# Kernel tuning notes

Measured on AMD Instinct MI355X. Metric: run time of the kernel, lower is better.

Reference implementation:

```python
import jax, jax.numpy as jnp
import numpy as np

D_MODEL = 1024
N_HEADS = 16
D_HEAD = D_MODEL // N_HEADS
ROPE_BASE = 10000.0


def _rotate_half(x):
    half = x.shape[-1] // 2
    x1, x2 = x[..., :half], x[..., half:]
    return jnp.concatenate([-x2, x1], axis=-1)


def _rope_cos_sin(seq_len, d_head, dtype):
    inv_freq = 1.0 / (ROPE_BASE ** (jnp.arange(0, d_head, 2, dtype=jnp.float32) / d_head))
    t = jnp.arange(seq_len, dtype=jnp.float32)
    freqs = jnp.outer(t, inv_freq)                       # [S, d_head/2]
    emb = jnp.concatenate([freqs, freqs], axis=-1)       # [S, d_head]
    return jnp.cos(emb).astype(dtype), jnp.sin(emb).astype(dtype)


def setup_inputs() -> dict:
    key = jax.random.key(0)
    k1, k2, k3 = jax.random.split(key, 3)
    B, S = 2, 2048
    x = jax.random.normal(k1, (B, S, D_MODEL), dtype=jnp.float32)
    # torch nn.Linear weight layout: [out_features, in_features], y = x @ W.T
    w_qkv = jax.random.normal(k2, (3 * D_MODEL, D_MODEL), dtype=jnp.float32) * (D_MODEL ** -0.5)
    w_out = jax.random.normal(k3, (D_MODEL, D_MODEL), dtype=jnp.float32) * (D_MODEL ** -0.5)
    return {"x": x, "w_qkv": w_qkv, "w_out": w_out}


def reference(x, w_qkv, w_out):
    B, S, _ = x.shape
    qkv = jnp.einsum('bsd,ed->bse', x, w_qkv)            # [B, S, 3*D]
    qkv = qkv.reshape(B, S, 3, N_HEADS, D_HEAD)
    qkv = jnp.transpose(qkv, (2, 0, 3, 1, 4))            # [3, B, H, S, Dh]
    q, k, v = qkv[0], qkv[1], qkv[2]

    cos, sin = _rope_cos_sin(S, D_HEAD, x.dtype)         # [S, Dh] each
    cos = cos[None, None]                                # [1, 1, S, Dh]
    sin = sin[None, None]
    q = q * cos + _rotate_half(q) * sin
    k = k * cos + _rotate_half(k) * sin

    scale = 1.0 / jnp.sqrt(jnp.array(D_HEAD, dtype=x.dtype))
    attn = jnp.einsum('bhqd,bhkd->bhqk', q, k) * scale   # [B, H, S, S]
    causal = jnp.tril(jnp.ones((S, S), dtype=bool))      # triu(diag=1) masked -> keep lower tri
    attn = jnp.where(causal[None, None], attn, jnp.finfo(x.dtype).min)
    attn = jax.nn.softmax(attn, axis=-1)

    out = jnp.einsum('bhqk,bhkd->bhqd', attn, v)         # [B, H, S, Dh]
    out = jnp.transpose(out, (0, 2, 1, 3)).reshape(B, S, D_MODEL)
    return jnp.einsum('bsd,ed->bse', out, w_out)         # out_proj
```

## Files before the change

### kernel.cpp

```cpp
#include <hip/hip_runtime.h>
#include <hip/hip_bf16.h>
#include <cmath>

#define DMODEL 1024
#define NH 16
#define DH 64
#define SEQ 2048
#define BATCH 2

typedef __attribute__((ext_vector_type(8))) short bf16x8;
typedef __attribute__((ext_vector_type(4))) float f32x4;
typedef __attribute__((ext_vector_type(4))) unsigned int u32x4;
typedef __attribute__((ext_vector_type(8))) unsigned short u16x8;

__device__ __forceinline__ unsigned short f2bf(float f) {
    unsigned int u = __builtin_bit_cast(unsigned int, f);
    u += 0x7fffu + ((u >> 16) & 1u);
    return (unsigned short)(u >> 16);
}
__device__ __forceinline__ float exp2_fast(float x) {
    float r;
    asm("v_exp_f32 %0, %1" : "=v"(r) : "v"(x));
    return r;
}

__global__ __launch_bounds__(256)
void cast_all(const float* __restrict__ x, const float* __restrict__ wq,
              const float* __restrict__ wo, unsigned short* __restrict__ xb,
              unsigned short* __restrict__ wqb, unsigned short* __restrict__ wob)
{
    const int i = blockIdx.x * 256 + threadIdx.x;
    const float* src; unsigned short* dst; int off;
    if (i < 524288)      { src = x;  dst = xb;  off = i; }
    else if (i < 917504) { src = wq; dst = wqb; off = i - 524288; }
    else                 { src = wo; dst = wob; off = i - 917504; }
    const float4 a = *(const float4*)(src + (size_t)off * 8);
    const float4 b = *(const float4*)(src + (size_t)off * 8 + 4);
    u16x8 o;
    o[0] = f2bf(a.x); o[1] = f2bf(a.y); o[2] = f2bf(a.z); o[3] = f2bf(a.w);
    o[4] = f2bf(b.x); o[5] = f2bf(b.y); o[6] = f2bf(b.z); o[7] = f2bf(b.w);
    *(u16x8*)(dst + (size_t)off * 8) = o;
}

template<int BM, int EPI>
__global__ __launch_bounds__(256)
void gemm_bf16(const unsigned short* __restrict__ A,
               const unsigned short* __restrict__ B,
               float* __restrict__ oc, unsigned short* __restrict__ oq,
               unsigned short* __restrict__ ok, unsigned short* __restrict__ ovt,
               int M, int N)
{
    constexpr int K = 1024;
    constexpr int BK = 32;
    constexpr int NT = K / BK;
    constexpr int FM = BM / 32;
    __shared__ unsigned short As[2][BM * BK];
    __shared__ unsigned short Bs[2][128 * BK];

    const int t  = threadIdx.x;
    const int l  = t & 63;
    const int w  = t >> 6;
    const int g  = l >> 4;
    const int ln = l & 15;
    const int wr = w >> 1, wc = w & 1;
    const int m0 = blockIdx.y * BM;
    const int n0 = blockIdx.x * 128;

    auto stage = [&](int kt, int bufi) {
        #pragma unroll
        for (int i = 0; i < BM / 64; ++i) {
            const int n = i * 256 + t;
            const int r = n >> 2, slot = n & 3;
            const int kk = kt * BK + ((slot ^ ((r >> 1) & 3)) * 8);
            const unsigned short* ga = A + (size_t)(m0 + r) * K + kk;
            __builtin_amdgcn_global_load_lds(
                (const __attribute__((address_space(1))) unsigned int*)ga,
                (__attribute__((address_space(3))) unsigned int*)&As[bufi][n * 8], 16, 0, 0);
        }
        #pragma unroll
        for (int i = 0; i < 2; ++i) {
            const int n = i * 256 + t;
            const int r = n >> 2, slot = n & 3;
            const int kk = kt * BK + ((slot ^ ((r >> 1) & 3)) * 8);
            const unsigned short* gb = B + (size_t)(n0 + r) * K + kk;
            __builtin_amdgcn_global_load_lds(
                (const __attribute__((address_space(1))) unsigned int*)gb,
                (__attribute__((address_space(3))) unsigned int*)&Bs[bufi][n * 8], 16, 0, 0);
        }
    };

    f32x4 acc[FM][4];
    #pragma unroll
    for (int i = 0; i < FM; ++i)
        #pragma unroll
        for (int j = 0; j < 4; ++j) acc[i][j] = (f32x4){0.f, 0.f, 0.f, 0.f};

    const int swz = (g ^ ((ln >> 1) & 3)) << 4;

    stage(0, 0);
    for (int kt = 0; kt < NT; ++kt) {
        __syncthreads();
        if (kt + 1 < NT) stage(kt + 1, (kt + 1) & 1);
        const char* as = (const char*)As[kt & 1];
        const char* bs = (const char*)Bs[kt & 1];
        bf16x8 af[FM], bfr[4];
        #pragma unroll
        for (int fm = 0; fm < FM; ++fm)
            af[fm] = *(const bf16x8*)(as + (wr * (BM / 2) + fm * 16 + ln) * 64 + swz);
        #pragma unroll
        for (int fn = 0; fn < 4; ++fn)
            bfr[fn] = *(const bf16x8*)(bs + (wc * 64 + fn * 16 + ln) * 64 + swz);
        #pragma unroll
        for (int fm = 0; fm < FM; ++fm)
            #pragma unroll
            for (int fn = 0; fn < 4; ++fn)
                acc[fm][fn] = __builtin_amdgcn_mfma_f32_16x16x32_bf16(
                    af[fm], bfr[fn], acc[fm][fn], 0, 0, 0);
    }

    const int rowbase = m0 + wr * (BM / 2);
    const int colbase = n0 + wc * 64;
    if (EPI == 1) {
        #pragma unroll
        for (int fm = 0; fm < FM; ++fm)
            #pragma unroll
            for (int fn = 0; fn < 4; ++fn)
                #pragma unroll
                for (int rr = 0; rr < 4; ++rr) {
                    const int row = rowbase + fm * 16 + g * 4 + rr;
                    oc[(size_t)row * N + colbase + fn * 16 + ln] = acc[fm][fn][rr];
                }
    } else {
        const int which = colbase >> 10;
        const int h = (colbase >> 6) & (NH - 1);
        if (which < 2) {
            unsigned short* dst = which == 0 ? oq : ok;
            const float scale = which == 0 ? 0.18033688011112042f : 1.f;
            const float cexp = -13.287712379549449f / 32.f;
            const float if0 = exp2f((float)ln * cexp);
            const float if1 = exp2f((float)(16 + ln) * cexp);
            #pragma unroll
            for (int fm = 0; fm < FM; ++fm)
                #pragma unroll
                for (int rr = 0; rr < 4; ++rr) {
                    const int row = rowbase + fm * 16 + g * 4 + rr;
                    const int b = row >> 11, s = row & (SEQ - 1);
                    float s0, c0, s1, c1;
                    __sincosf((float)s * if0, &s0, &c0);
                    __sincosf((float)s * if1, &s1, &c1);
                    const float x0 = acc[fm][0][rr], x1 = acc[fm][1][rr];
                    const float x2 = acc[fm][2][rr], x3 = acc[fm][3][rr];
                    const size_t base = (((size_t)b * NH + h) * SEQ + s) * DH;
                    dst[base + ln]      = f2bf((x0 * c0 - x2 * s0) * scale);
                    dst[base + 16 + ln] = f2bf((x1 * c1 - x3 * s1) * scale);
                    dst[base + 32 + ln] = f2bf((x2 * c0 + x0 * s0) * scale);
                    dst[base + 48 + ln] = f2bf((x3 * c1 + x1 * s1) * scale);
                }
        } else {
            #pragma unroll
            for (int fm = 0; fm < FM; ++fm)
                #pragma unroll
                for (int fn = 0; fn < 4; ++fn) {
                    const int row = rowbase + fm * 16 + g * 4;
                    const int b = row >> 11, s = row & (SEQ - 1);
                    const int d = fn * 16 + ln;
                    ushort4 pk;
                    pk.x = f2bf(acc[fm][fn][0]); pk.y = f2bf(acc[fm][fn][1]);
                    pk.z = f2bf(acc[fm][fn][2]); pk.w = f2bf(acc[fm][fn][3]);
                    *(ushort4*)&ovt[(((size_t)b * NH + h) * DH + d) * SEQ + s] = pk;
                }
        }
    }
}

__global__ __launch_bounds__(512)
void attn_mfma(const unsigned short* __restrict__ q,
               const unsigned short* __restrict__ k,
               const unsigned short* __restrict__ vt,
               unsigned short* __restrict__ ob)
{
    __shared__ unsigned short Ks[2][64 * 64];
    __shared__ unsigned short Vs[2][64 * 64];

    const int t  = threadIdx.x;
    const int l  = t & 63;
    const int w  = t >> 6;
    const int wq = w & 3;
    const int g  = l >> 4;
    const int ln = l & 15;
    const int bid = blockIdx.x;
    const int xcd = bid & 7, jj = bid >> 3;
    const int bh = xcd * 4 + (jj >> 4);
    const int pi = jj & 15;
    const int qtA = pi, qtB = 31 - pi;
    const int myqt = (w < 4) ? qtA : qtB;
    const size_t bqk = (size_t)bh * SEQ * DH;
    const size_t bv  = (size_t)bh * DH * SEQ;

    bf16x8 qf0, qf1;
    {
        const unsigned short* qp = q + bqk + (size_t)(myqt * 64 + wq * 16 + ln) * DH + g * 8;
        qf0 = *(const bf16x8*)qp;
        qf1 = *(const bf16x8*)(qp + 32);
    }

    f32x4 ao[4];
    #pragma unroll
    for (int i = 0; i < 4; ++i) ao[i] = (f32x4){0.f, 0.f, 0.f, 0.f};
    float l_ = 0.f;

    auto stage = [&](int kt, int bufi) {
        const int row = t >> 3, sl = t & 7;
        const int sg  = (row & 3) | (((row >> 3) & 1) << 2);
        const int slg = (sl ^ sg) * 8;
        const unsigned short* gk = k  + bqk + (size_t)(kt * 64 + row) * DH + slg;
        const unsigned short* gv = vt + bv  + (size_t)row * SEQ + kt * 64 + slg;
        __builtin_amdgcn_global_load_lds(
            (const __attribute__((address_space(1))) unsigned int*)gk,
            (__attribute__((address_space(3))) unsigned int*)&Ks[bufi][t * 8], 16, 0, 0);
        __builtin_amdgcn_global_load_lds(
            (const __attribute__((address_space(1))) unsigned int*)gv,
            (__attribute__((address_space(3))) unsigned int*)&Vs[bufi][t * 8], 16, 0, 0);
    };

    const int rowoffK = ((ln >> 2) * 8 + (ln & 3)) * 128;
    const int sK = (ln & 3) | (((ln >> 2) & 1) << 2);
    const int slotK0 = ((g ^ sK) << 4);
    const int slotK1 = (((g + 4) ^ sK) << 4);
    const int sV = (ln & 3) | (((ln >> 3) & 1) << 2);

    stage(0, 0);
    for (int kt = 0; kt <= qtB; ++kt) {
        __syncthreads();
        if (kt < qtB) stage(kt + 1, (kt + 1) & 1);
        const bool act = (kt <= myqt);
        const char* kb = (const char*)Ks[kt & 1];
        const char* vb = (const char*)Vs[kt & 1];

        if (act) {
            f32x4 s[4];
            #pragma unroll
            for (int nb = 0; nb < 4; ++nb) s[nb] = (f32x4){0.f, 0.f, 0.f, 0.f};

            __builtin_amdgcn_s_setprio(1);
            #pragma unroll
            for (int nb = 0; nb < 4; ++nb) {
                const char* kr = kb + ((nb >> 1) * 32 + (nb & 1) * 4) * 128 + rowoffK;
                bf16x8 kf0 = *(const bf16x8*)(kr + slotK0);
                bf16x8 kf1 = *(const bf16x8*)(kr + slotK1);
                s[nb] = __builtin_amdgcn_mfma_f32_16x16x32_bf16(kf0, qf0, s[nb], 0, 0, 0);
                s[nb] = __builtin_amdgcn_mfma_f32_16x16x32_bf16(kf1, qf1, s[nb], 0, 0, 0);
            }
            __builtin_amdgcn_s_setprio(0);

            if (kt == myqt) {
                #pragma unroll
                for (int nb = 0; nb < 4; ++nb)
                    #pragma unroll
                    for (int r = 0; r < 4; ++r)
                        if ((nb >> 1) * 32 + g * 8 + (nb & 1) * 4 + r > wq * 16 + ln)
                            s[nb][r] = -INFINITY;
            }

            const float M2 = 28.853900817779268f;
            bf16x8 pf[2];
            {
                float rs = 0.f;
                unsigned int dw[8];
                #pragma unroll
                for (int nb = 0; nb < 4; ++nb) {
                    float e[4];
                    #pragma unroll
                    for (int r = 0; r < 4; ++r)
                        e[r] = exp2_fast(s[nb][r] - M2);
                    rs += (e[0] + e[1]) + (e[2] + e[3]);
                    dw[nb * 2] = __builtin_amdgcn_perm(
                        __builtin_bit_cast(unsigned int, e[1]),
                        __builtin_bit_cast(unsigned int, e[0]), 0x07060302u);
                    dw[nb * 2 + 1] = __builtin_amdgcn_perm(
                        __builtin_bit_cast(unsigned int, e[3]),
                        __builtin_bit_cast(unsigned int, e[2]), 0x07060302u);
                }
                l_ += rs;
                pf[0] = __builtin_bit_cast(bf16x8, (u32x4){dw[0], dw[1], dw[2], dw[3]});
                pf[1] = __builtin_bit_cast(bf16x8, (u32x4){dw[4], dw[5], dw[6], dw[7]});
            }

            __builtin_amdgcn_s_setprio(1);
            #pragma unroll
            for (int ks = 0; ks < 2; ++ks) {
                #pragma unroll
                for (int db = 0; db < 4; ++db) {
                    const int d = db * 16 + ln;
                    bf16x8 vf = *(const bf16x8*)(vb + d * 128 + (((ks * 4 + g) ^ sV) << 4));
                    ao[db] = __builtin_amdgcn_mfma_f32_16x16x32_bf16(pf[ks], vf, ao[db], 0, 0, 0);
                }
            }
            __builtin_amdgcn_s_setprio(0);
        }
    }

    l_ += __shfl_xor(l_, 16); l_ += __shfl_xor(l_, 32);
    const int b = bh >> 4, h = bh & (NH - 1);
    const float inv = 1.f / l_;
    #pragma unroll
    for (int r = 0; r < 4; ++r) {
        const float iv = __shfl(inv, g * 4 + r);
        const size_t row = (size_t)(b * SEQ + myqt * 64 + wq * 16 + g * 4 + r) * DMODEL + h * DH;
        #pragma unroll
        for (int db = 0; db < 4; ++db)
            ob[row + db * 16 + ln] = f2bf(ao[db][r] * iv);
    }
}

extern "C" void kernel_launch(void* const* d_in, const int* in_sizes, int n_in,
                              void* d_out, int out_size, void* d_ws, size_t ws_size,
                              hipStream_t stream)
{
    const float* x  = (const float*)d_in[0];
    const float* wq = (const float*)d_in[1];
    const float* wo = (const float*)d_in[2];
    float* out = (float*)d_out;

    const size_t NQ = (size_t)BATCH * NH * SEQ * DH;
    unsigned short* qb  = (unsigned short*)d_ws;
    unsigned short* kb  = qb + NQ;
    unsigned short* vtb = kb + NQ;
    unsigned short* ob  = vtb + NQ;
    unsigned short* xb  = ob + NQ;
    unsigned short* wqb = xb + NQ;
    unsigned short* wob = wqb + 3 * DMODEL * DMODEL;

    cast_all<<<4096, 256, 0, stream>>>(x, wq, wo, xb, wqb, wob);

    dim3 g1(3072 / 128, 4096 / 128);
    gemm_bf16<128, 0><<<g1, 256, 0, stream>>>(xb, wqb, nullptr, qb, kb, vtb, 4096, 3072);

    attn_mfma<<<512, 512, 0, stream>>>(qb, kb, vtb, ob);

    dim3 g3(1024 / 128, 4096 / 64);
    gemm_bf16<64, 1><<<g3, 256, 0, stream>>>(ob, wob, out, nullptr, nullptr, nullptr, 4096, 1024);
}
```

Measured before the change: 107.5 us.

## Process two query sub-tiles per wave in attention and remap GEMM blocks per XCD

The attention kernel now gives each wave 32 query rows as two 16-row MFMA tiles that share the same K and V fragment loads, and each block covers four query tiles (balanced causal pairs j, 31-j, j+8, 23-j). This halves the attention grid to 256 blocks while doubling the per-wave MFMA work for each LDS read. Both GEMMs switch to a 1D grid with XCD-aware block mapping, so blocks on the same XCD share column tiles of the weight matrix for L2 reuse. The cost is higher register pressure from the extra accumulators and fewer blocks, which may leave some CUs idle with only 256 attention blocks.

Result: slower. 119.6 us (+11.2%).

```diff
diff --git a/kernel.cpp b/kernel.cpp
--- a/kernel.cpp
+++ b/kernel.cpp
@@ -63,8 +63,15 @@
     const int g  = l >> 4;
     const int ln = l & 15;
     const int wr = w >> 1, wc = w & 1;
-    const int m0 = blockIdx.y * BM;
-    const int n0 = blockIdx.x * 128;
+
+    const int nbc = N >> 7;
+    const int cpx = nbc >> 3;
+    const int bid = blockIdx.x;
+    const int xcd = bid & 7, rr2 = bid >> 3;
+    const int nb = xcd * cpx + (rr2 % cpx);
+    const int mb = rr2 / cpx;
+    const int m0 = mb * BM;
+    const int n0 = nb * 128;
 
     auto stage = [&](int kt, int bufi) {
         #pragma unroll
@@ -185,29 +192,36 @@
     const int t  = threadIdx.x;
     const int l  = t & 63;
     const int w  = t >> 6;
-    const int wq = w & 3;
     const int g  = l >> 4;
     const int ln = l & 15;
     const int bid = blockIdx.x;
-    const int xcd = bid & 7, jj = bid >> 3;
-    const int bh = xcd * 4 + (jj >> 4);
-    const int pi = jj & 15;
-    const int qtA = pi, qtB = 31 - pi;
-    const int myqt = (w < 4) ? qtA : qtB;
+    const int xcd = bid & 7;
+    const int rem = bid >> 3;
+    const int bh  = xcd * 4 + (rem >> 3);
+    const int j   = rem & 7;
+    const int tidx = w >> 1;
+    const int myqt = (tidx == 0) ? j : (tidx == 1) ? (31 - j)
+                   : (tidx == 2) ? (j + 8) : (23 - j);
+    const int qtMax = 31 - j;
+    const int half = (w & 1) * 32;
     const size_t bqk = (size_t)bh * SEQ * DH;
     const size_t bv  = (size_t)bh * DH * SEQ;
 
-    bf16x8 qf0, qf1;
+    bf16x8 qf00, qf01, qf10, qf11;
     {
-        const unsigned short* qp = q + bqk + (size_t)(myqt * 64 + wq * 16 + ln) * DH + g * 8;
-        qf0 = *(const bf16x8*)qp;
-        qf1 = *(const bf16x8*)(qp + 32);
-    }
-
-    f32x4 ao[4];
+        const unsigned short* qp0 = q + bqk + (size_t)(myqt * 64 + half + ln) * DH + g * 8;
+        qf00 = *(const bf16x8*)qp0;  qf01 = *(const bf16x8*)(qp0 + 32);
+        const unsigned short* qp1 = q + bqk + (size_t)(myqt * 64 + half + 16 + ln) * DH + g * 8;
+        qf10 = *(const bf16x8*)qp1;  qf11 = *(const bf16x8*)(qp1 + 32);
+    }
+
+    f32x4 ao0[4], ao1[4];
     #pragma unroll
-    for (int i = 0; i < 4; ++i) ao[i] = (f32x4){0.f, 0.f, 0.f, 0.f};
-    float l_ = 0.f;
+    for (int i = 0; i < 4; ++i) {
+        ao0[i] = (f32x4){0.f, 0.f, 0.f, 0.f};
+        ao1[i] = (f32x4){0.f, 0.f, 0.f, 0.f};
+    }
+    float l0 = 0.f, l1 = 0.f;
 
     auto stage = [&](int kt, int bufi) {
         const int row = t >> 3, sl = t & 7;
@@ -229,18 +243,44 @@
     const int slotK1 = (((g + 4) ^ sK) << 4);
     const int sV = (ln & 3) | (((ln >> 3) & 1) << 2);
 
+    auto softmax_tile = [&](f32x4* s, float& l_, bf16x8* pf) {
+        const float M2 = 28.853900817779268f;
+        float rs = 0.f;
+        unsigned int dw[8];
+        #pragma unroll
+        for (int nb = 0; nb < 4; ++nb) {
+            float e[4];
+            #pragma unroll
+            for (int r = 0; r < 4; ++r)
+                e[r] = exp2_fast(s[nb][r] - M2);
+            rs += (e[0] + e[1]) + (e[2] + e[3]);
+            dw[nb * 2] = __builtin_amdgcn_perm(
+                __builtin_bit_cast(unsigned int, e[1]),
+                __builtin_bit_cast(unsigned int, e[0]), 0x07060302u);
+            dw[nb * 2 + 1] = __builtin_amdgcn_perm(
+                __builtin_bit_cast(unsigned int, e[3]),
+                __builtin_bit_cast(unsigned int, e[2]), 0x07060302u);
+        }
+        l_ += rs;
+        pf[0] = __builtin_bit_cast(bf16x8, (u32x4){dw[0], dw[1], dw[2], dw[3]});
+        pf[1] = __builtin_bit_cast(bf16x8, (u32x4){dw[4], dw[5], dw[6], dw[7]});
+    };
+
     stage(0, 0);
-    for (int kt = 0; kt <= qtB; ++kt) {
+    for (int kt = 0; kt <= qtMax; ++kt) {
         __syncthreads();
-        if (kt < qtB) stage(kt + 1, (kt + 1) & 1);
+        if (kt < qtMax) stage(kt + 1, (kt + 1) & 1);
         const bool act = (kt <= myqt);
         const char* kb = (const char*)Ks[kt & 1];
         const char* vb = (const char*)Vs[kt & 1];
 
         if (act) {
-            f32x4 s[4];
-            #pragma unroll
-            for (int nb = 0; nb < 4; ++nb) s[nb] = (f32x4){0.f, 0.f, 0.f, 0.f};
+            f32x4 s0[4], s1[4];
+            #pragma unroll
+            for (int nb = 0; nb < 4; ++nb) {
+                s0[nb] = (f32x4){0.f, 0.f, 0.f, 0.f};
+                s1[nb] = (f32x4){0.f, 0.f, 0.f, 0.f};
+            }
 
             __builtin_amdgcn_s_setprio(1);
             #pragma unroll
@@ -248,8 +288,10 @@
                 const char* kr = kb + ((nb >> 1) * 32 + (nb & 1) * 4) * 128 + rowoffK;
                 bf16x8 kf0 = *(const bf16x8*)(kr + slotK0);
                 bf16x8 kf1 = *(const bf16x8*)(kr + slotK1);
-                s[nb] = __builtin_amdgcn_mfma_f32_16x16x32_bf16(kf0, qf0, s[nb], 0, 0, 0);
-                s[nb] = __builtin_amdgcn_mfma_f32_16x16x32_bf16(kf1, qf1, s[nb], 0, 0, 0);
+                s0[nb] = __builtin_amdgcn_mfma_f32_16x16x32_bf16(kf0, qf00, s0[nb], 0, 0, 0);
+                s0[nb] = __builtin_amdgcn_mfma_f32_16x16x32_bf16(kf1, qf01, s0[nb], 0, 0, 0);
+                s1[nb] = __builtin_amdgcn_mfma_f32_16x16x32_bf16(kf0, qf10, s1[nb], 0, 0, 0);
+                s1[nb] = __builtin_amdgcn_mfma_f32_16x16x32_bf16(kf1, qf11, s1[nb], 0, 0, 0);
             }
             __builtin_amdgcn_s_setprio(0);
 
@@ -257,34 +299,16 @@
                 #pragma unroll
                 for (int nb = 0; nb < 4; ++nb)
                     #pragma unroll
-                    for (int r = 0; r < 4; ++r)
-                        if ((nb >> 1) * 32 + g * 8 + (nb & 1) * 4 + r > wq * 16 + ln)
-                            s[nb][r] = -INFINITY;
+                    for (int r = 0; r < 4; ++r) {
+                        const int key = (nb >> 1) * 32 + g * 8 + (nb & 1) * 4 + r;
+                        if (key > half + ln)      s0[nb][r] = -INFINITY;
+                        if (key > half + 16 + ln) s1[nb][r] = -INFINITY;
+                    }
             }
 
-            const float M2 = 28.853900817779268f;
-            bf16x8 pf[2];
-            {
-                float rs = 0.f;
-                unsigned int dw[8];
-                #pragma unroll
-                for (int nb = 0; nb < 4; ++nb) {
-                    float e[4];
-                    #pragma unroll
-                    for (int r = 0; r < 4; ++r)
-                        e[r] = exp2_fast(s[nb][r] - M2);
-                    rs += (e[0] + e[1]) + (e[2] + e[3]);
-                    dw[nb * 2] = __builtin_amdgcn_perm(
-                        __builtin_bit_cast(unsigned int, e[1]),
-                        __builtin_bit_cast(unsigned int, e[0]), 0x07060302u);
-                    dw[nb * 2 + 1] = __builtin_amdgcn_perm(
-                        __builtin_bit_cast(unsigned int, e[3]),
-                        __builtin_bit_cast(unsigned int, e[2]), 0x07060302u);
-                }
-                l_ += rs;
-                pf[0] = __builtin_bit_cast(bf16x8, (u32x4){dw[0], dw[1], dw[2], dw[3]});
-                pf[1] = __builtin_bit_cast(bf16x8, (u32x4){dw[4], dw[5], dw[6], dw[7]});
-            }
+            bf16x8 pf0[2], pf1[2];
+            softmax_tile(s0, l0, pf0);
+            softmax_tile(s1, l1, pf1);
 
             __builtin_amdgcn_s_setprio(1);
             #pragma unroll
@@ -293,23 +317,29 @@
                 for (int db = 0; db < 4; ++db) {
                     const int d = db * 16 + ln;
                     bf16x8 vf = *(const bf16x8*)(vb + d * 128 + (((ks * 4 + g) ^ sV) << 4));
-                    ao[db] = __builtin_amdgcn_mfma_f32_16x16x32_bf16(pf[ks], vf, ao[db], 0, 0, 0);
+                    ao0[db] = __builtin_amdgcn_mfma_f32_16x16x32_bf16(pf0[ks], vf, ao0[db], 0, 0, 0);
+                    ao1[db] = __builtin_amdgcn_mfma_f32_16x16x32_bf16(pf1[ks], vf, ao1[db], 0, 0, 0);
                 }
             }
             __builtin_amdgcn_s_setprio(0);
         }
     }
 
-    l_ += __shfl_xor(l_, 16); l_ += __shfl_xor(l_, 32);
+    l0 += __shfl_xor(l0, 16); l0 += __shfl_xor(l0, 32);
+    l1 += __shfl_xor(l1, 16); l1 += __shfl_xor(l1, 32);
     const int b = bh >> 4, h = bh & (NH - 1);
-    const float inv = 1.f / l_;
+    const float inv0 = 1.f / l0, inv1 = 1.f / l1;
     #pragma unroll
     for (int r = 0; r < 4; ++r) {
-        const float iv = __shfl(inv, g * 4 + r);
-        const size_t row = (size_t)(b * SEQ + myqt * 64 + wq * 16 + g * 4 + r) * DMODEL + h * DH;
-        #pragma unroll
-        for (int db = 0; db < 4; ++db)
-            ob[row + db * 16 + ln] = f2bf(ao[db][r] * iv);
+        const float iv0 = __shfl(inv0, g * 4 + r);
+        const float iv1 = __shfl(inv1, g * 4 + r);
+        const size_t row0 = (size_t)(b * SEQ + myqt * 64 + half + g * 4 + r) * DMODEL + h * DH;
+        const size_t row1 = (size_t)(b * SEQ + myqt * 64 + half + 16 + g * 4 + r) * DMODEL + h * DH;
+        #pragma unroll
+        for (int db = 0; db < 4; ++db) {
+            ob[row0 + db * 16 + ln] = f2bf(ao0[db][r] * iv0);
+            ob[row1 + db * 16 + ln] = f2bf(ao1[db][r] * iv1);
+        }
     }
 }
 
@@ -333,11 +363,9 @@
 
     cast_all<<<4096, 256, 0, stream>>>(x, wq, wo, xb, wqb, wob);
 
-    dim3 g1(3072 / 128, 4096 / 128);
-    gemm_bf16<128, 0><<<g1, 256, 0, stream>>>(xb, wqb, nullptr, qb, kb, vtb, 4096, 3072);
-
-    attn_mfma<<<512, 512, 0, stream>>>(qb, kb, vtb, ob);
-
-    dim3 g3(1024 / 128, 4096 / 64);
-    gemm_bf16<64, 1><<<g3, 256, 0, stream>>>(ob, wob, out, nullptr, nullptr, nullptr, 4096, 1024);
-}
+    gemm_bf16<128, 0><<<768, 256, 0, stream>>>(xb, wqb, nullptr, qb, kb, vtb, 4096, 3072);
+
+    attn_mfma<<<256, 512, 0, stream>>>(qb, kb, vtb, ob);
+
+    gemm_bf16<64, 1><<<512, 256, 0, stream>>>(ob, wob, out, nullptr, nullptr, nullptr, 4096, 1024);
+}
```
